# Optimization experiments

Hardware: AMD Instinct MI355X
Metric: run time of the kernel (lower is better)

## Reference

```python
import jax, jax.numpy as jnp
import numpy as np

M_FEATS = 1536      # number of proposals (docstring: [M, K])
K_DIM = 128         # feature dim per docstring example
NUM_CLASSES = 16    # label vocabulary; torch.unique loop becomes a fixed class sweep


def setup_inputs() -> dict:
    key = jax.random.key(0)
    k1, k2 = jax.random.split(key)
    features = jax.random.normal(k1, (M_FEATS, K_DIM), dtype=jnp.float32)
    labels = jax.random.randint(k2, (M_FEATS,), 0, NUM_CLASSES, dtype=jnp.int32)
    # ious all ones -> keep = (ious >= 0.5) is all-True, so the boolean filter is identity
    ious = jnp.ones((M_FEATS,), dtype=jnp.float32)
    return {"features": features, "labels": labels, "ious": ious}


def reference(features, labels, ious):
    # reweight_func='none' -> coef = ones_like(ious); keep mask is all-True by construction
    coef = jnp.ones_like(ious)
    # similarity [M, M]; coef broadcasts over columns, matching `similarity * coef` in torch
    sim = jnp.matmul(features, features.T) * coef[None, :]
    m = sim.shape[0]
    eye = jnp.eye(m, dtype=sim.dtype)
    # ground set term: logdet(similarity + 0.5 I)  (mask_ground is all ones)
    ground = jnp.linalg.slogdet(sim + 0.5 * eye)[1]

    # Per-label logdet of the submatrix S_c + 0.5 I_{n_c}. Instead of extracting a
    # variable-size submatrix (not jit-able), embed it in a full [M, M] matrix that is
    # block-diagonal: class block = S_c + 0.5 I, off-class diagonal = 1. Its logdet
    # equals logdet(S_c + 0.5 I). Absent classes give identity -> logdet 0, matching
    # torch.unique skipping them.
    onehot = (labels[:, None] == jnp.arange(NUM_CLASSES, dtype=labels.dtype)[None, :])
    onehot = onehot.astype(sim.dtype)  # [M, C]

    def class_logdet(mask):  # mask: [M] 0/1 indicator for one class
        A = sim * (mask[:, None] * mask[None, :]) + jnp.diag(0.5 * mask + (1.0 - mask))
        return jnp.linalg.slogdet(A)[1]

    per_class = jax.vmap(class_logdet)(onehot.T)  # [C]
    loss = jnp.sum(per_class) - ground
    return loss  # scalar; .mean() of a scalar is itself
```

## Files before the change

### kernel.cpp

```cpp
#include <hip/hip_runtime.h>
#include <math.h>


#define M_FEATS 1536
#define K_DIM 128
#define NUM_CLASSES 16
#define SLICE 96
#define GRAM_ELEMS (K_DIM * K_DIM)
#define PIDX(i) ((i) + ((i) >> 4))
#define SENT 0x13579BDF

__device__ __forceinline__ float chol128(
    float A[8][8], const int t, const int rg, const int cg,
    const int i0, const int j0,
    float4* panLo, float4* panHi, float4* wshLo, float4* wshHi, float* logp)
{
    if (rg == 0) {
#pragma unroll
        for (int q = 0; q < 8; ++q) {
            panLo[PIDX(j0 + q)] = make_float4(A[0][q], A[1][q], A[2][q], A[3][q]);
            panHi[PIDX(j0 + q)] = make_float4(A[4][q], A[5][q], A[6][q], A[7][q]);
        }
    }

#pragma unroll 1
    for (int s = 0; s < 16; ++s) {
        const int k = 8 * s;
        __syncthreads();

        if (t < K_DIM) {
            float4 dL[8], dH[8];
#pragma unroll
            for (int c = 0; c < 8; ++c) {
                dL[c] = panLo[PIDX(k + c)];
                dH[c] = panHi[PIDX(k + c)];
            }
            float4 aL = panLo[PIDX(t)], aH = panHi[PIDX(t)];

            float D[8][8];
#pragma unroll
            for (int c = 0; c < 8; ++c) {
                D[0][c] = dL[c].x; D[1][c] = dL[c].y;
                D[2][c] = dL[c].z; D[3][c] = dL[c].w;
                D[4][c] = dH[c].x; D[5][c] = dH[c].y;
                D[6][c] = dH[c].z; D[7][c] = dH[c].w;
            }

            float L[8][8], ic[8];
            float prod = 1.0f;
#pragma unroll
            for (int c = 0; c < 8; ++c) {
                float v = D[c][c];
#pragma unroll
                for (int m = 0; m < c; ++m) v = fmaf(-L[c][m], L[c][m], v);
                prod *= v;
                ic[c] = rsqrtf(v);
#pragma unroll
                for (int r = c + 1; r < 8; ++r) {
                    float x = D[r][c];
#pragma unroll
                    for (int m = 0; m < c; ++m) x = fmaf(-L[r][m], L[c][m], x);
                    L[r][c] = x * ic[c];
                }
            }
            if (t == 0) logp[s] = prod;

            float a[8] = {aL.x, aL.y, aL.z, aL.w, aH.x, aH.y, aH.z, aH.w};
            float w[8];
#pragma unroll
            for (int c = 0; c < 8; ++c) {
                float x = a[c];
#pragma unroll
                for (int m = 0; m < c; ++m) x = fmaf(-L[c][m], w[m], x);
                w[c] = x * ic[c];
            }
            wshLo[PIDX(t)] = make_float4(w[0], w[1], w[2], w[3]);
            wshHi[PIDX(t)] = make_float4(w[4], w[5], w[6], w[7]);
        }
        __syncthreads();

        if (rg > s && cg > s) {
            float4 wrL[8], wrH[8];
#pragma unroll
            for (int r = 0; r < 8; ++r) {
                wrL[r] = wshLo[PIDX(i0 + r)];
                wrH[r] = wshHi[PIDX(i0 + r)];
            }
#pragma unroll
            for (int q = 0; q < 8; ++q) {
                float4 wjL = wshLo[PIDX(j0 + q)];
                float4 wjH = wshHi[PIDX(j0 + q)];
#pragma unroll
                for (int r = 0; r < 8; ++r) {
                    float x = A[r][q];
                    x = fmaf(-wrL[r].x, wjL.x, x);
                    x = fmaf(-wrL[r].y, wjL.y, x);
                    x = fmaf(-wrL[r].z, wjL.z, x);
                    x = fmaf(-wrL[r].w, wjL.w, x);
                    x = fmaf(-wrH[r].x, wjH.x, x);
                    x = fmaf(-wrH[r].y, wjH.y, x);
                    x = fmaf(-wrH[r].z, wjH.z, x);
                    x = fmaf(-wrH[r].w, wjH.w, x);
                    A[r][q] = x;
                }
            }
        }
        if (rg == s + 1) {
#pragma unroll
            for (int q = 0; q < 8; ++q) {
                panLo[PIDX(j0 + q)] = make_float4(A[0][q], A[1][q], A[2][q], A[3][q]);
                panHi[PIDX(j0 + q)] = make_float4(A[4][q], A[5][q], A[6][q], A[7][q]);
            }
        }
    }

    float ls = 0.0f;
    if (t == 0) {
#pragma unroll
        for (int s = 0; s < 16; ++s) ls += logf(logp[s]);
    }
    return ls;
}

__global__ __launch_bounds__(256, 1) void fused_kernel(
    const float* __restrict__ f, const int* __restrict__ labels,
    float* __restrict__ partials, float* __restrict__ groundG,
    int* __restrict__ flag1, int* __restrict__ flag2,
    float* __restrict__ ldet, int* __restrict__ flag3,
    float* __restrict__ out)
{
    __shared__ int cnt;
    __shared__ int list[M_FEATS];
    __shared__ float4 panLo[136], panHi[136], wshLo[136], wshHi[136];
    __shared__ float logp[16];

    const int b = blockIdx.x;
    const int t = threadIdx.x;
    const int rg = t >> 4;
    const int cg = t & 15;
    const int i0 = rg << 3;
    const int j0 = cg << 3;

    float A[8][8];

    if (b < NUM_CLASSES) {
#pragma unroll
        for (int r = 0; r < 8; ++r)
#pragma unroll
            for (int q = 0; q < 8; ++q) A[r][q] = 0.0f;

        const float* base = f + (size_t)(SLICE * b) * K_DIM;
        float4 A0[6], A1[6], B0[6], B1[6];
#pragma unroll
        for (int u = 0; u < 6; ++u) {
            const float* rp = base + (size_t)u * K_DIM;
            A0[u] = *(const float4*)(rp + i0);
            A1[u] = *(const float4*)(rp + i0 + 4);
            B0[u] = *(const float4*)(rp + j0);
            B1[u] = *(const float4*)(rp + j0 + 4);
        }
        for (int jb = 0; jb < SLICE; jb += 6) {
#pragma unroll
            for (int u = 0; u < 6; ++u) {
                float fa[8] = {A0[u].x, A0[u].y, A0[u].z, A0[u].w,
                               A1[u].x, A1[u].y, A1[u].z, A1[u].w};
                float fb[8] = {B0[u].x, B0[u].y, B0[u].z, B0[u].w,
                               B1[u].x, B1[u].y, B1[u].z, B1[u].w};
#pragma unroll
                for (int r = 0; r < 8; ++r)
#pragma unroll
                    for (int q = 0; q < 8; ++q)
                        A[r][q] = fmaf(fa[r], fb[q], A[r][q]);
                int p = jb + u + 6;
                const float* rp = base + (size_t)(p < SLICE ? p : SLICE - 1) * K_DIM;
                A0[u] = *(const float4*)(rp + i0);
                A1[u] = *(const float4*)(rp + i0 + 4);
                B0[u] = *(const float4*)(rp + j0);
                B1[u] = *(const float4*)(rp + j0 + 4);
            }
        }

        float* g = partials + (size_t)b * GRAM_ELEMS;
#pragma unroll
        for (int r = 0; r < 8; ++r) {
            *(float4*)(g + (i0 + r) * K_DIM + j0) =
                make_float4(A[r][0], A[r][1], A[r][2], A[r][3]);
            *(float4*)(g + (i0 + r) * K_DIM + j0 + 4) =
                make_float4(A[r][4], A[r][5], A[r][6], A[r][7]);
        }
        __syncthreads();
        if (t == 0)
            __hip_atomic_store(&flag1[b], SENT, __ATOMIC_RELEASE,
                               __HIP_MEMORY_SCOPE_AGENT);

        if (t < NUM_CLASSES)
            while (__hip_atomic_load(&flag1[t], __ATOMIC_ACQUIRE,
                                     __HIP_MEMORY_SCOPE_AGENT) != SENT)
                __builtin_amdgcn_s_sleep(2);
        __syncthreads();

        {
            const int row = 8 * b + (t >> 5);
            const int col = (t & 31) << 2;
            float4 s = make_float4(0.f, 0.f, 0.f, 0.f);
#pragma unroll
            for (int c = 0; c < NUM_CLASSES; ++c) {
                float4 v = *(const float4*)(partials + (size_t)c * GRAM_ELEMS
                                            + row * K_DIM + col);
                s.x += v.x; s.y += v.y; s.z += v.z; s.w += v.w;
            }
            *(float4*)(groundG + row * K_DIM + col) = s;
        }
        __syncthreads();
        if (t == 0)
            __hip_atomic_store(&flag2[b], SENT, __ATOMIC_RELEASE,
                               __HIP_MEMORY_SCOPE_AGENT);
        return;
    }

    if (b < 2 * NUM_CLASSES) {
        const int cls = b - NUM_CLASSES;
        if (t == 0) cnt = 0;
        __syncthreads();

        {
            const int lane = t & 63;
            const unsigned long long ltmask = (lane == 63)
                ? 0x7FFFFFFFFFFFFFFFull : ((1ull << lane) - 1ull);
#pragma unroll
            for (int it = 0; it < M_FEATS / 256; ++it) {
                const int i = it * 256 + t;
                const bool pred = (labels[i] == cls);
                const unsigned long long mask = __ballot(pred);
                int base = 0;
                if (lane == 0 && mask)
                    base = atomicAdd(&cnt, __popcll(mask));
                base = __shfl(base, 0);
                if (pred)
                    list[base + __popcll(mask & ltmask)] = i;
            }
        }
        __syncthreads();
        const int n = cnt;

#pragma unroll
        for (int r = 0; r < 8; ++r)
#pragma unroll
            for (int q = 0; q < 8; ++q) A[r][q] = 0.0f;

        if (n > 0) {
            float4 A0[6], A1[6], B0[6], B1[6];
            int lidx[6];
#pragma unroll
            for (int u = 0; u < 6; ++u) {
                const float* rp = f + (size_t)list[u < n ? u : n - 1] * K_DIM;
                A0[u] = *(const float4*)(rp + i0);
                A1[u] = *(const float4*)(rp + i0 + 4);
                B0[u] = *(const float4*)(rp + j0);
                B1[u] = *(const float4*)(rp + j0 + 4);
                const int p = u + 6;
                lidx[u] = list[p < n ? p : n - 1];
            }
            for (int jb = 0; jb < n; jb += 6) {
#pragma unroll
                for (int u = 0; u < 6; ++u) {
                    if (jb + u < n) {
                        float fa[8] = {A0[u].x, A0[u].y, A0[u].z, A0[u].w,
                                       A1[u].x, A1[u].y, A1[u].z, A1[u].w};
                        float fb[8] = {B0[u].x, B0[u].y, B0[u].z, B0[u].w,
                                       B1[u].x, B1[u].y, B1[u].z, B1[u].w};
#pragma unroll
                        for (int r = 0; r < 8; ++r)
#pragma unroll
                            for (int q = 0; q < 8; ++q)
                                A[r][q] = fmaf(fa[r], fb[q], A[r][q]);
                    }
                    const float* rp = f + (size_t)lidx[u] * K_DIM;
                    A0[u] = *(const float4*)(rp + i0);
                    A1[u] = *(const float4*)(rp + i0 + 4);
                    B0[u] = *(const float4*)(rp + j0);
                    B1[u] = *(const float4*)(rp + j0 + 4);
                    const int p = jb + u + 12;
                    lidx[u] = list[p < n ? p : n - 1];
                }
            }
        }

#pragma unroll
        for (int r = 0; r < 8; ++r)
#pragma unroll
            for (int q = 0; q < 8; ++q)
                if ((i0 + r) == (j0 + q)) A[r][q] += 0.5f;

        float ls = chol128(A, t, rg, cg, i0, j0, panLo, panHi, wshLo, wshHi, logp);

        if (t == 0) {
            ldet[cls] = ls;
            __hip_atomic_store(&flag3[cls], SENT, __ATOMIC_RELEASE,
                               __HIP_MEMORY_SCOPE_AGENT);
        }
        return;
    }

    if (t < NUM_CLASSES)
        while (__hip_atomic_load(&flag2[t], __ATOMIC_ACQUIRE,
                                 __HIP_MEMORY_SCOPE_AGENT) != SENT)
            __builtin_amdgcn_s_sleep(2);
    __syncthreads();

#pragma unroll
    for (int r = 0; r < 8; ++r) {
        float4 v0 = *(const float4*)(groundG + (i0 + r) * K_DIM + j0);
        float4 v1 = *(const float4*)(groundG + (i0 + r) * K_DIM + j0 + 4);
        A[r][0] = v0.x; A[r][1] = v0.y; A[r][2] = v0.z; A[r][3] = v0.w;
        A[r][4] = v1.x; A[r][5] = v1.y; A[r][6] = v1.z; A[r][7] = v1.w;
    }
#pragma unroll
    for (int r = 0; r < 8; ++r)
#pragma unroll
        for (int q = 0; q < 8; ++q)
            if ((i0 + r) == (j0 + q)) A[r][q] += 0.5f;

    float ls = chol128(A, t, rg, cg, i0, j0, panLo, panHi, wshLo, wshHi, logp);

    if (t < NUM_CLASSES)
        while (__hip_atomic_load(&flag3[t], __ATOMIC_ACQUIRE,
                                 __HIP_MEMORY_SCOPE_AGENT) != SENT)
            __builtin_amdgcn_s_sleep(2);
    __syncthreads();

    if (t == 0) {
        float total = 1920.0f * 0.6931471805599453f - ls;
#pragma unroll
        for (int c = 0; c < NUM_CLASSES; ++c) total += ldet[c];
        out[0] = total;
    }
}

extern "C" void kernel_launch(void* const* d_in, const int* in_sizes, int n_in,
                              void* d_out, int out_size, void* d_ws, size_t ws_size,
                              hipStream_t stream)
{
    const float* features = (const float*)d_in[0];
    const int* labels = (const int*)d_in[1];

    float* partials = (float*)d_ws;
    float* groundG  = partials + (size_t)NUM_CLASSES * GRAM_ELEMS;
    int* flag1      = (int*)(groundG + GRAM_ELEMS);
    int* flag2      = flag1 + NUM_CLASSES;
    float* ldetp    = (float*)(flag2 + NUM_CLASSES);
    int* flag3      = (int*)(ldetp + NUM_CLASSES);

    fused_kernel<<<2 * NUM_CLASSES + 1, 256, 0, stream>>>(
        features, labels, partials, groundG, flag1, flag2, ldetp, flag3,
        (float*)d_out);
}
```

Measured before the change: 103.9 us.

## Compute Gram matrices with bf16 MFMA via shared-memory transposed staging

Replaces the per-thread fp32 FMA outer-product Gram accumulation (for both the ground slices and the per-class gathers) with a shared MFMA routine. Each 96-row chunk is converted to bf16, staged transposed in LDS, and multiplied with 16x16x32 bf16 matrix instructions. Per-class Grams now go through a global scratch buffer and are read back into the Cholesky register layout. This trades fp32 precision for matrix-core throughput, which risks logdet accuracy, and adds an extra global round trip plus LDS staging and barriers.

```diff
diff --git a/kernel.cpp b/kernel.cpp
--- a/kernel.cpp
+++ b/kernel.cpp
@@ -9,6 +9,76 @@
 #define GRAM_ELEMS (K_DIM * K_DIM)
 #define PIDX(i) ((i) + ((i) >> 4))
 #define SENT 0x13579BDF
+#define MP 104
+
+typedef short bf16x8 __attribute__((ext_vector_type(8)));
+typedef float f32x4 __attribute__((ext_vector_type(4)));
+
+__device__ __forceinline__ short f2bf(float x) {
+    unsigned u = __float_as_uint(x);
+    u += 0x7FFFu + ((u >> 16) & 1u);
+    return (short)(u >> 16);
+}
+
+__device__ __forceinline__ void gram_mfma(
+    const float* __restrict__ f, const int* list, int n, int contig_base,
+    short* FT, float* __restrict__ gout, int t)
+{
+    const int wave = t >> 6, lane = t & 63, ln = lane & 15, quad = lane >> 4;
+    const int mlane = t & 31, cgrp = t >> 5;
+
+    f32x4 acc[2][8];
+#pragma unroll
+    for (int x = 0; x < 2; ++x)
+#pragma unroll
+        for (int tc = 0; tc < 8; ++tc)
+            acc[x][tc] = (f32x4){0.f, 0.f, 0.f, 0.f};
+
+    const int nchunks = (n + 95) / 96;
+    for (int ch = 0; ch < nchunks; ++ch) {
+        const int cb = ch * 96;
+#pragma unroll
+        for (int it = 0; it < 12; ++it) {
+            const int m = (it % 3) * 32 + mlane;
+            const int cg = (it / 3) * 8 + cgrp;
+            const int gm = cb + m;
+            float4 v = make_float4(0.f, 0.f, 0.f, 0.f);
+            if (gm < n) {
+                const int src = list ? list[gm] : (contig_base + gm);
+                v = *(const float4*)(f + (size_t)src * K_DIM + cg * 4);
+            }
+            FT[(cg * 4 + 0) * MP + m] = f2bf(v.x);
+            FT[(cg * 4 + 1) * MP + m] = f2bf(v.y);
+            FT[(cg * 4 + 2) * MP + m] = f2bf(v.z);
+            FT[(cg * 4 + 3) * MP + m] = f2bf(v.w);
+        }
+        __syncthreads();
+#pragma unroll
+        for (int kc = 0; kc < 3; ++kc) {
+            const int kb = kc * 32 + quad * 8;
+            bf16x8 a0 = *(const bf16x8*)(FT + ((wave * 2 + 0) * 16 + ln) * MP + kb);
+            bf16x8 a1 = *(const bf16x8*)(FT + ((wave * 2 + 1) * 16 + ln) * MP + kb);
+#pragma unroll
+            for (int tc = 0; tc < 8; ++tc) {
+                bf16x8 bb = *(const bf16x8*)(FT + (tc * 16 + ln) * MP + kb);
+                acc[0][tc] = __builtin_amdgcn_mfma_f32_16x16x32_bf16(
+                    a0, bb, acc[0][tc], 0, 0, 0);
+                acc[1][tc] = __builtin_amdgcn_mfma_f32_16x16x32_bf16(
+                    a1, bb, acc[1][tc], 0, 0, 0);
+            }
+        }
+        __syncthreads();
+    }
+
+#pragma unroll
+    for (int x = 0; x < 2; ++x)
+#pragma unroll
+        for (int tc = 0; tc < 8; ++tc)
+#pragma unroll
+            for (int rr = 0; rr < 4; ++rr)
+                gout[((wave * 2 + x) * 16 + quad * 4 + rr) * K_DIM + tc * 16 + ln]
+                    = acc[x][tc][rr];
+}
 
 __device__ __forceinline__ float chol128(
     float A[8][8], const int t, const int rg, const int cg,
@@ -125,12 +195,14 @@
 __global__ __launch_bounds__(256, 1) void fused_kernel(
     const float* __restrict__ f, const int* __restrict__ labels,
     float* __restrict__ partials, float* __restrict__ groundG,
+    float* __restrict__ cgrams,
     int* __restrict__ flag1, int* __restrict__ flag2,
     float* __restrict__ ldet, int* __restrict__ flag3,
     float* __restrict__ out)
 {
     __shared__ int cnt;
     __shared__ int list[M_FEATS];
+    __shared__ short FT[K_DIM * MP];
     __shared__ float4 panLo[136], panHi[136], wshLo[136], wshHi[136];
     __shared__ float logp[16];
 
@@ -144,50 +216,8 @@
     float A[8][8];
 
     if (b < NUM_CLASSES) {
-#pragma unroll
-        for (int r = 0; r < 8; ++r)
-#pragma unroll
-            for (int q = 0; q < 8; ++q) A[r][q] = 0.0f;
-
-        const float* base = f + (size_t)(SLICE * b) * K_DIM;
-        float4 A0[6], A1[6], B0[6], B1[6];
-#pragma unroll
-        for (int u = 0; u < 6; ++u) {
-            const float* rp = base + (size_t)u * K_DIM;
-            A0[u] = *(const float4*)(rp + i0);
-            A1[u] = *(const float4*)(rp + i0 + 4);
-            B0[u] = *(const float4*)(rp + j0);
-            B1[u] = *(const float4*)(rp + j0 + 4);
-        }
-        for (int jb = 0; jb < SLICE; jb += 6) {
-#pragma unroll
-            for (int u = 0; u < 6; ++u) {
-                float fa[8] = {A0[u].x, A0[u].y, A0[u].z, A0[u].w,
-                               A1[u].x, A1[u].y, A1[u].z, A1[u].w};
-                float fb[8] = {B0[u].x, B0[u].y, B0[u].z, B0[u].w,
-                               B1[u].x, B1[u].y, B1[u].z, B1[u].w};
-#pragma unroll
-                for (int r = 0; r < 8; ++r)
-#pragma unroll
-                    for (int q = 0; q < 8; ++q)
-                        A[r][q] = fmaf(fa[r], fb[q], A[r][q]);
-                int p = jb + u + 6;
-                const float* rp = base + (size_t)(p < SLICE ? p : SLICE - 1) * K_DIM;
-                A0[u] = *(const float4*)(rp + i0);
-                A1[u] = *(const float4*)(rp + i0 + 4);
-                B0[u] = *(const float4*)(rp + j0);
-                B1[u] = *(const float4*)(rp + j0 + 4);
-            }
-        }
-
-        float* g = partials + (size_t)b * GRAM_ELEMS;
-#pragma unroll
-        for (int r = 0; r < 8; ++r) {
-            *(float4*)(g + (i0 + r) * K_DIM + j0) =
-                make_float4(A[r][0], A[r][1], A[r][2], A[r][3]);
-            *(float4*)(g + (i0 + r) * K_DIM + j0 + 4) =
-                make_float4(A[r][4], A[r][5], A[r][6], A[r][7]);
-        }
+        gram_mfma(f, nullptr, SLICE, SLICE * b, FT,
+                  partials + (size_t)b * GRAM_ELEMS, t);
         __syncthreads();
         if (t == 0)
             __hip_atomic_store(&flag1[b], SENT, __ATOMIC_RELEASE,
@@ -222,7 +252,6 @@
         const int cls = b - NUM_CLASSES;
         if (t == 0) cnt = 0;
         __syncthreads();
-
         {
             const int lane = t & 63;
             const unsigned long long ltmask = (lane == 63)
@@ -243,49 +272,17 @@
         __syncthreads();
         const int n = cnt;
 
-#pragma unroll
-        for (int r = 0; r < 8; ++r)
-#pragma unroll
-            for (int q = 0; q < 8; ++q) A[r][q] = 0.0f;
-
-        if (n > 0) {
-            float4 A0[6], A1[6], B0[6], B1[6];
-            int lidx[6];
-#pragma unroll
-            for (int u = 0; u < 6; ++u) {
-                const float* rp = f + (size_t)list[u < n ? u : n - 1] * K_DIM;
-                A0[u] = *(const float4*)(rp + i0);
-                A1[u] = *(const float4*)(rp + i0 + 4);
-                B0[u] = *(const float4*)(rp + j0);
-                B1[u] = *(const float4*)(rp + j0 + 4);
-                const int p = u + 6;
-                lidx[u] = list[p < n ? p : n - 1];
-            }
-            for (int jb = 0; jb < n; jb += 6) {
-#pragma unroll
-                for (int u = 0; u < 6; ++u) {
-                    if (jb + u < n) {
-                        float fa[8] = {A0[u].x, A0[u].y, A0[u].z, A0[u].w,
-                                       A1[u].x, A1[u].y, A1[u].z, A1[u].w};
-                        float fb[8] = {B0[u].x, B0[u].y, B0[u].z, B0[u].w,
-                                       B1[u].x, B1[u].y, B1[u].z, B1[u].w};
-#pragma unroll
-                        for (int r = 0; r < 8; ++r)
-#pragma unroll
-                            for (int q = 0; q < 8; ++q)
-                                A[r][q] = fmaf(fa[r], fb[q], A[r][q]);
-                    }
-                    const float* rp = f + (size_t)lidx[u] * K_DIM;
-                    A0[u] = *(const float4*)(rp + i0);
-                    A1[u] = *(const float4*)(rp + i0 + 4);
-                    B0[u] = *(const float4*)(rp + j0);
-                    B1[u] = *(const float4*)(rp + j0 + 4);
-                    const int p = jb + u + 12;
-                    lidx[u] = list[p < n ? p : n - 1];
-                }
-            }
-        }
-
+        float* g = cgrams + (size_t)cls * GRAM_ELEMS;
+        gram_mfma(f, list, n, 0, FT, g, t);
+        __syncthreads();
+
+#pragma unroll
+        for (int r = 0; r < 8; ++r) {
+            float4 v0 = *(const float4*)(g + (i0 + r) * K_DIM + j0);
+            float4 v1 = *(const float4*)(g + (i0 + r) * K_DIM + j0 + 4);
+            A[r][0] = v0.x; A[r][1] = v0.y; A[r][2] = v0.z; A[r][3] = v0.w;
+            A[r][4] = v1.x; A[r][5] = v1.y; A[r][6] = v1.z; A[r][7] = v1.w;
+        }
 #pragma unroll
         for (int r = 0; r < 8; ++r)
 #pragma unroll
@@ -346,12 +343,13 @@
 
     float* partials = (float*)d_ws;
     float* groundG  = partials + (size_t)NUM_CLASSES * GRAM_ELEMS;
-    int* flag1      = (int*)(groundG + GRAM_ELEMS);
+    float* cgrams   = groundG + GRAM_ELEMS;
+    int* flag1      = (int*)(cgrams + (size_t)NUM_CLASSES * GRAM_ELEMS);
     int* flag2      = flag1 + NUM_CLASSES;
     float* ldetp    = (float*)(flag2 + NUM_CLASSES);
     int* flag3      = (int*)(ldetp + NUM_CLASSES);
 
     fused_kernel<<<2 * NUM_CLASSES + 1, 256, 0, stream>>>(
-        features, labels, partials, groundG, flag1, flag2, ldetp, flag3,
+        features, labels, partials, groundG, cgrams, flag1, flag2, ldetp, flag3,
         (float*)d_out);
 }
```

After: 97.09 us. 1.07x faster.
